# Performance work log

Hardware: AMD Instinct MI355X
Metric: run time of the kernel (lower is better)

The kernel has to match this reference:

```python
import jax, jax.numpy as jnp
import numpy as np
from jax import lax

N, D = 32768, 512
N_Q, BINS = 8, 2048


def setup_inputs() -> dict:
    key = jax.random.key(0)
    k1, k2 = jax.random.split(key)
    hidden_states = jax.random.normal(k1, (N, D), dtype=jnp.float32)
    # learned codebooks: n_q stages, each [BINS, D] (bins list clamps to one size)
    codebooks = jax.random.normal(k2, (N_Q, BINS, D), dtype=jnp.float32)
    return {"hidden_states": hidden_states, "codebooks": codebooks}


def reference(hidden_states, codebooks):
    """ResidualVectorQuantizer.encode: sequential residual VQ over n_q codebooks.

    Distances sum((r - c)^2) computed via the GEMM expansion
    ||r||^2 - 2 r.c^T + ||c||^2 (same math, matmul-friendly).
    Returns (codes [n_q, N] int, quantized [N, D]).
    """
    cb_sq = jnp.sum(codebooks * codebooks, axis=-1)  # [n_q, bins]

    def step(carry, stage):
        residual, quantized = carry
        cb, csq = stage  # [bins, D], [bins]
        r_sq = jnp.sum(residual * residual, axis=-1, keepdims=True)  # [N, 1]
        dist = r_sq - 2.0 * (residual @ cb.T) + csq[None, :]  # [N, bins]
        idx = jnp.argmin(dist, axis=-1)  # [N]
        chosen = cb[idx]  # [N, D]
        return (residual - chosen, quantized + chosen), idx

    init = (hidden_states, jnp.zeros_like(hidden_states))
    (_, quantized), codes = lax.scan(step, init, (codebooks, cb_sq))
    return codes, quantized
```

## Files before the change

kernel.cpp:

```cpp
#include <hip/hip_runtime.h>
#include <hip/hip_bf16.h>

#define NROWS 32768
#define DIM   512
#define NQ    8
#define NBINS 2048

#define MARGIN 1.0f

typedef __attribute__((ext_vector_type(8))) short short8v;
typedef __attribute__((ext_vector_type(4))) float f32x4;

__device__ inline unsigned short f2bf(float x) {
    __hip_bfloat16 h = __float2bfloat16(x);
    return *reinterpret_cast<unsigned short*>(&h);
}

typedef __attribute__((address_space(3))) void lds_t;
typedef __attribute__((address_space(1))) const void gbl_t;
__device__ inline void gload16(const void* g, void* l) {
    __builtin_amdgcn_global_load_lds((gbl_t*)g, (lds_t*)l, 16, 0, 0);
}

__device__ inline float pw_combine(float s) {
#pragma unroll
    for (int m = 1; m <= 16; m <<= 1) {
        float o = __shfl_xor(s, m, 64);
        s = __fadd_rn(s, o);
    }
    return s;
}

__global__ __launch_bounds__(256) void k_prep(const float* __restrict__ cb,
                                              unsigned short* __restrict__ o,
                                              float* __restrict__ csq32) {
    int row = blockIdx.x * 4 + (threadIdx.x >> 6);
    int lane = threadIdx.x & 63;
    const float* cp = cb + (size_t)row * DIM;

    float4 a = *(const float4*)(cp + lane * 8);
    float4 b = *(const float4*)(cp + lane * 8 + 4);
    short8v v;
    v[0] = f2bf(a.x); v[1] = f2bf(a.y); v[2] = f2bf(a.z); v[3] = f2bf(a.w);
    v[4] = f2bf(b.x); v[5] = f2bf(b.y); v[6] = f2bf(b.z); v[7] = f2bf(b.w);
    *(short8v*)(o + (size_t)row * DIM + lane * 8) = v;

    float s = 0.0f;
    if (lane < 32) {
        int base = (lane >> 3) * 128 + (lane & 7);
        float e = cp[base];
        s = __fmul_rn(e, e);
#pragma unroll
        for (int m = 1; m < 16; ++m) {
            float e2 = cp[base + 8 * m];
            s = __fadd_rn(s, __fmul_rn(e2, e2));
        }
    }
    s = pw_combine(s);
    if (lane == 0) csq32[row] = s;
}

__global__ __launch_bounds__(128) void k_init(const float* __restrict__ h,
                                              float* __restrict__ rout,
                                              float* __restrict__ rsq,
                                              unsigned short* __restrict__ ahi) {
    int row = blockIdx.x;
    int t = threadIdx.x;
    __shared__ float sq[DIM];
    float4 r = *(const float4*)(h + (size_t)row * DIM + t * 4);
    *(float4*)(rout + (size_t)row * DIM + t * 4) = r;
    ushort4 hv;
    hv.x = f2bf(r.x); hv.y = f2bf(r.y); hv.z = f2bf(r.z); hv.w = f2bf(r.w);
    *(ushort4*)(ahi + (size_t)row * DIM + t * 4) = hv;
    sq[t * 4 + 0] = __fmul_rn(r.x, r.x);
    sq[t * 4 + 1] = __fmul_rn(r.y, r.y);
    sq[t * 4 + 2] = __fmul_rn(r.z, r.z);
    sq[t * 4 + 3] = __fmul_rn(r.w, r.w);
    __syncthreads();
    if (t < 32) {
        int base = (t >> 3) * 128 + (t & 7);
        float s = sq[base];
#pragma unroll
        for (int m = 1; m < 16; ++m) s = __fadd_rn(s, sq[base + 8 * m]);
        s = pw_combine(s);
        if (t == 0) rsq[row] = s;
    }
}

__global__ __launch_bounds__(256, 4) void k_gemm(const unsigned short* __restrict__ Ahi,
                                                 const unsigned short* __restrict__ Bcb,
                                                 const float* __restrict__ csq,
                                                 float* __restrict__ partD,
                                                 int* __restrict__ partI) {
    __shared__ __align__(16) char lds[33792];
    __shared__ float csqS[128];

    const int tid = threadIdx.x;
    const int lane = tid & 63;
    const int w = tid >> 6;
    const int wr = w >> 1;
    const int wc = w & 1;

    const int wg = blockIdx.x;
    const int rem = wg & 255;
    const int panel = (rem & 7) * 32 + (rem >> 3);
    const int T = wg >> 8;

    if (tid < 128) csqS[tid] = csq[T * 128 + tid];

    const char* Abase = (const char*)(Ahi + (size_t)panel * 128 * DIM);
    const char* Bbase = (const char*)(Bcb + (size_t)T * 128 * DIM);

    int goff[4], loff[4];
#pragma unroll
    for (int i = 0; i < 4; ++i) {
        int L = i * 256 + tid;
        int row = L >> 3, cc = L & 7;
        goff[i] = row * (DIM * 2) + ((cc ^ (row & 7)) << 4);
        loff[i] = L * 16;
    }

    f32x4 acc[4][4];
#pragma unroll
    for (int m = 0; m < 4; ++m)
#pragma unroll
        for (int n = 0; n < 4; ++n) acc[m][n] = (f32x4){0.f, 0.f, 0.f, 0.f};

#pragma unroll
    for (int ks = 0; ks < 8; ++ks) {
        __syncthreads();
        const int k0b = ks * 128;
#pragma unroll
        for (int i = 0; i < 4; ++i) {
            gload16(Abase + goff[i] + k0b, lds + loff[i]);
            gload16(Bbase + goff[i] + k0b, lds + 16384 + loff[i]);
        }
        __syncthreads();
        __builtin_amdgcn_s_setprio(1);
        const char* Ab = lds;
        const char* Bb = lds + 16384;
#pragma unroll
        for (int kk = 0; kk < 2; ++kk) {
            const int sw = (((kk * 4 + (lane >> 4)) ^ (lane & 7)) << 4);
            short8v bF[4];
#pragma unroll
            for (int n = 0; n < 4; ++n) {
                int rowB = wc * 64 + n * 16 + (lane & 15);
                bF[n] = *(const short8v*)(Bb + rowB * 128 + sw);
            }
#pragma unroll
            for (int m = 0; m < 4; ++m) {
                int rowA = wr * 64 + m * 16 + (lane & 15);
                short8v aF = *(const short8v*)(Ab + rowA * 128 + sw);
#pragma unroll
                for (int n = 0; n < 4; ++n)
                    acc[m][n] = __builtin_amdgcn_mfma_f32_16x16x32_bf16(
                        aF, bF[n], acc[m][n], 0, 0, 0);
            }
        }
        __builtin_amdgcn_s_setprio(0);
    }

    float td0 = 3.4e38f, td1 = 3.4e38f, td2 = 3.4e38f, td3 = 3.4e38f;
    int ti0 = 0, ti1 = 0, ti2 = 0, ti3 = 0;
    float* distf = (float*)lds;
    const int row2 = tid >> 1, h = tid & 1;

#pragma unroll
    for (int p = 0; p < 2; ++p) {
        __syncthreads();
        if (wc == p) {
#pragma unroll
            for (int m = 0; m < 4; ++m)
#pragma unroll
                for (int n = 0; n < 4; ++n)
#pragma unroll
                    for (int r = 0; r < 4; ++r) {
                        int row = wr * 64 + m * 16 + (lane >> 4) * 4 + r;
                        int cl = n * 16 + (lane & 15);
                        distf[row * 66 + cl] = csqS[p * 64 + cl] - 2.0f * acc[m][n][r];
                    }
        }
        __syncthreads();
        int binb = T * 128 + p * 64 + h * 32;
        for (int c = 0; c < 32; ++c) {
            float d = distf[row2 * 66 + h * 32 + c];
            int bin = binb + c;
            if (d < td3) {
                if (d < td2) {
                    td3 = td2; ti3 = ti2;
                    if (d < td1) {
                        td2 = td1; ti2 = ti1;
                        if (d < td0) { td1 = td0; ti1 = ti0; td0 = d; ti0 = bin; }
                        else { td1 = d; ti1 = bin; }
                    } else { td2 = d; ti2 = bin; }
                } else { td3 = d; ti3 = bin; }
            }
        }
    }
#pragma unroll
    for (int j = 0; j < 4; ++j) {
        float d = __shfl_xor(j == 0 ? td0 : (j == 1 ? td1 : (j == 2 ? td2 : td3)), 1);
        int bin = __shfl_xor(j == 0 ? ti0 : (j == 1 ? ti1 : (j == 2 ? ti2 : ti3)), 1);
        if (d < td3) {
            if (d < td2) {
                td3 = td2; ti3 = ti2;
                if (d < td1) {
                    td2 = td1; ti2 = ti1;
                    if (d < td0) { td1 = td0; ti1 = ti0; td0 = d; ti0 = bin; }
                    else { td1 = d; ti1 = bin; }
                } else { td2 = d; ti2 = bin; }
            } else { td3 = d; ti3 = bin; }
        }
    }
    if (h == 0) {
        size_t g = ((size_t)panel * 128 + row2) * 64 + T * 4;
        partD[g + 0] = td0; partI[g + 0] = ti0;
        partD[g + 1] = td1; partI[g + 1] = ti1;
        partD[g + 2] = td2; partI[g + 2] = ti2;
        partD[g + 3] = td3; partI[g + 3] = ti3;
    }
}

__global__ __launch_bounds__(128) void k_ru(const float* __restrict__ partD,
                                            const int* __restrict__ partI,
                                            float* __restrict__ resid,
                                            float* __restrict__ rsq,
                                            const float* __restrict__ csq,
                                            const float* __restrict__ cb,
                                            float* __restrict__ codeOut,
                                            unsigned short* __restrict__ ahi,
                                            const float* __restrict__ hidden,
                                            int last) {
    const int row = blockIdx.x;
    const int t = threadIdx.x;
    __shared__ int sIdx;
    __shared__ float sq[DIM];

    if (t < 64) {
        float d = partD[(size_t)row * 64 + t];
        int bi0 = partI[(size_t)row * 64 + t];

        float bd = d; int bix = bi0;
#pragma unroll
        for (int o = 32; o > 0; o >>= 1) {
            float od = __shfl_xor(bd, o);
            int oi = __shfl_xor(bix, o);
            if (od < bd || (od == bd && oi < bix)) { bd = od; bix = oi; }
        }
        bool cand = (d <= bd + MARGIN);
        unsigned long long mask = __ballot(cand);
        int winI;
        if (__popcll(mask) == 1) {
            winI = bix;
        } else {
            float myD = 3.4e38f; int myI = 0x7fffffff;
            if (cand) {
                const float* rp = resid + (size_t)row * DIM;
                const float* cp = cb + (size_t)bi0 * DIM;
                float acc = 0.0f;
                for (int k = 0; k < DIM; k += 4) {
                    float4 rv = *(const float4*)(rp + k);
                    float4 cv = *(const float4*)(cp + k);
                    acc = fmaf(rv.x, cv.x, acc);
                    acc = fmaf(rv.y, cv.y, acc);
                    acc = fmaf(rv.z, cv.z, acc);
                    acc = fmaf(rv.w, cv.w, acc);
                }
                myD = __fadd_rn(__fsub_rn(rsq[row], __fmul_rn(2.0f, acc)), csq[bi0]);
                myI = bi0;
            }
#pragma unroll
            for (int o = 32; o > 0; o >>= 1) {
                float od = __shfl_xor(myD, o);
                int oi = __shfl_xor(myI, o);
                if (od < myD || (od == myD && oi < myI)) { myD = od; myI = oi; }
            }
            winI = myI;
        }
        if (t == 0) {
            sIdx = winI;
            codeOut[row] = (float)winI;
        }
    }
    __syncthreads();
    const int id = sIdx;

    float4 r = *(const float4*)(resid + (size_t)row * DIM + t * 4);
    float4 c = *(const float4*)(cb + (size_t)id * DIM + t * 4);
    r.x = __fsub_rn(r.x, c.x);
    r.y = __fsub_rn(r.y, c.y);
    r.z = __fsub_rn(r.z, c.z);
    r.w = __fsub_rn(r.w, c.w);

    if (last) {
        float4 hv4 = *(const float4*)(hidden + (size_t)row * DIM + t * 4);
        float4 q;
        q.x = __fsub_rn(hv4.x, r.x);
        q.y = __fsub_rn(hv4.y, r.y);
        q.z = __fsub_rn(hv4.z, r.z);
        q.w = __fsub_rn(hv4.w, r.w);
        *(float4*)(resid + (size_t)row * DIM + t * 4) = q;
        return;
    }

    *(float4*)(resid + (size_t)row * DIM + t * 4) = r;
    ushort4 hv;
    hv.x = f2bf(r.x); hv.y = f2bf(r.y); hv.z = f2bf(r.z); hv.w = f2bf(r.w);
    *(ushort4*)(ahi + (size_t)row * DIM + t * 4) = hv;

    sq[t * 4 + 0] = __fmul_rn(r.x, r.x);
    sq[t * 4 + 1] = __fmul_rn(r.y, r.y);
    sq[t * 4 + 2] = __fmul_rn(r.z, r.z);
    sq[t * 4 + 3] = __fmul_rn(r.w, r.w);
    __syncthreads();
    if (t < 32) {
        int base = (t >> 3) * 128 + (t & 7);
        float s = sq[base];
#pragma unroll
        for (int m = 1; m < 16; ++m) s = __fadd_rn(s, sq[base + 8 * m]);
        s = pw_combine(s);
        if (t == 0) rsq[row] = s;
    }
}

extern "C" void kernel_launch(void* const* d_in, const int* in_sizes, int n_in,
                              void* d_out, int out_size, void* d_ws, size_t ws_size,
                              hipStream_t stream) {
    const float* hidden = (const float*)d_in[0];
    const float* cbs = (const float*)d_in[1];

    float* out_codes = (float*)d_out;
    float* resid = out_codes + (size_t)NQ * NROWS;

    unsigned short* Ahi = (unsigned short*)d_ws;
    unsigned short* Cbf = Ahi + (size_t)NROWS * DIM;
    float* csq32 = (float*)(Cbf + (size_t)NQ * NBINS * DIM);
    float* rsq = csq32 + (size_t)NQ * NBINS;
    float* partD = rsq + NROWS;
    int* partI = (int*)(partD + (size_t)NROWS * 64);

    k_prep<<<NQ * NBINS / 4, 256, 0, stream>>>(cbs, Cbf, csq32);
    k_init<<<NROWS, 128, 0, stream>>>(hidden, resid, rsq, Ahi);

    for (int s = 0; s < NQ; ++s) {
        const float* cbS = cbs + (size_t)s * NBINS * DIM;
        k_gemm<<<(NROWS / 128) * (NBINS / 128), 256, 0, stream>>>(
            Ahi, Cbf + (size_t)s * NBINS * DIM, csq32 + (size_t)s * NBINS,
            partD, partI);
        k_ru<<<NROWS, 128, 0, stream>>>(partD, partI, resid, rsq,
                                        csq32 + (size_t)s * NBINS, cbS,
                                        out_codes + (size_t)s * NROWS, Ahi,
                                        hidden, s == NQ - 1);
    }
}
```

Measured before the change: 1.219 ms.

## Remap GEMM workgroup order and process one row per wavefront in update kernel

The GEMM block-index mapping is changed so each group of consecutive workgroups covers a 16-panel by 16-codebook-tile region, which should improve L2 reuse of the A panels and B tiles. The residual-update kernel now gives each 64-lane wavefront a whole row (4 rows per 256-thread block) instead of one 128-thread block per row. This removes the shared-memory index broadcast and the first block barrier, and the residual load is issued early so it overlaps the argmin reduction. Each lane now handles 8 elements with wider bf16 stores. The rsq reduction keeps the same summation order, so results should be unchanged.

```diff
diff --git a/kernel.cpp b/kernel.cpp
--- a/kernel.cpp
+++ b/kernel.cpp
@@ -102,9 +102,9 @@
     const int wc = w & 1;
 
     const int wg = blockIdx.x;
-    const int rem = wg & 255;
-    const int panel = (rem & 7) * 32 + (rem >> 3);
-    const int T = wg >> 8;
+    const int seq = wg >> 3;
+    const int panel = (wg & 7) * 32 + (seq >> 8) * 16 + (seq & 15);
+    const int T = (seq >> 4) & 15;
 
     if (tid < 128) csqS[tid] = csq[T * 128 + tid];
 
@@ -222,7 +222,7 @@
     }
 }
 
-__global__ __launch_bounds__(128) void k_ru(const float* __restrict__ partD,
+__global__ __launch_bounds__(256) void k_ru(const float* __restrict__ partD,
                                             const int* __restrict__ partI,
                                             float* __restrict__ resid,
                                             float* __restrict__ rsq,
@@ -232,95 +232,110 @@
                                             unsigned short* __restrict__ ahi,
                                             const float* __restrict__ hidden,
                                             int last) {
-    const int row = blockIdx.x;
-    const int t = threadIdx.x;
-    __shared__ int sIdx;
-    __shared__ float sq[DIM];
-
-    if (t < 64) {
-        float d = partD[(size_t)row * 64 + t];
-        int bi0 = partI[(size_t)row * 64 + t];
-
-        float bd = d; int bix = bi0;
+    const int w = threadIdx.x >> 6;
+    const int lane = threadIdx.x & 63;
+    const int row = blockIdx.x * 4 + w;
+    __shared__ float sq[4][DIM];
+
+    const float* rp = resid + (size_t)row * DIM;
+    float4 r0 = *(const float4*)(rp + lane * 8);
+    float4 r1 = *(const float4*)(rp + lane * 8 + 4);
+
+    float d = partD[(size_t)row * 64 + lane];
+    int bi0 = partI[(size_t)row * 64 + lane];
+    float bd = d; int bix = bi0;
+#pragma unroll
+    for (int o = 32; o > 0; o >>= 1) {
+        float od = __shfl_xor(bd, o);
+        int oi = __shfl_xor(bix, o);
+        if (od < bd || (od == bd && oi < bix)) { bd = od; bix = oi; }
+    }
+    bool cand = (d <= bd + MARGIN);
+    unsigned long long mask = __ballot(cand);
+    int winI;
+    if (__popcll(mask) == 1) {
+        winI = bix;
+    } else {
+        float myD = 3.4e38f; int myI = 0x7fffffff;
+        if (cand) {
+            const float* cp = cb + (size_t)bi0 * DIM;
+            float acc = 0.0f;
+            for (int k = 0; k < DIM; k += 4) {
+                float4 rv = *(const float4*)(rp + k);
+                float4 cv = *(const float4*)(cp + k);
+                acc = fmaf(rv.x, cv.x, acc);
+                acc = fmaf(rv.y, cv.y, acc);
+                acc = fmaf(rv.z, cv.z, acc);
+                acc = fmaf(rv.w, cv.w, acc);
+            }
+            myD = __fadd_rn(__fsub_rn(rsq[row], __fmul_rn(2.0f, acc)), csq[bi0]);
+            myI = bi0;
+        }
 #pragma unroll
         for (int o = 32; o > 0; o >>= 1) {
-            float od = __shfl_xor(bd, o);
-            int oi = __shfl_xor(bix, o);
-            if (od < bd || (od == bd && oi < bix)) { bd = od; bix = oi; }
-        }
-        bool cand = (d <= bd + MARGIN);
-        unsigned long long mask = __ballot(cand);
-        int winI;
-        if (__popcll(mask) == 1) {
-            winI = bix;
-        } else {
-            float myD = 3.4e38f; int myI = 0x7fffffff;
-            if (cand) {
-                const float* rp = resid + (size_t)row * DIM;
-                const float* cp = cb + (size_t)bi0 * DIM;
-                float acc = 0.0f;
-                for (int k = 0; k < DIM; k += 4) {
-                    float4 rv = *(const float4*)(rp + k);
-                    float4 cv = *(const float4*)(cp + k);
-                    acc = fmaf(rv.x, cv.x, acc);
-                    acc = fmaf(rv.y, cv.y, acc);
-                    acc = fmaf(rv.z, cv.z, acc);
-                    acc = fmaf(rv.w, cv.w, acc);
-                }
-                myD = __fadd_rn(__fsub_rn(rsq[row], __fmul_rn(2.0f, acc)), csq[bi0]);
-                myI = bi0;
-            }
-#pragma unroll
-            for (int o = 32; o > 0; o >>= 1) {
-                float od = __shfl_xor(myD, o);
-                int oi = __shfl_xor(myI, o);
-                if (od < myD || (od == myD && oi < myI)) { myD = od; myI = oi; }
-            }
-            winI = myI;
-        }
-        if (t == 0) {
-            sIdx = winI;
-            codeOut[row] = (float)winI;
-        }
-    }
+            float od = __shfl_xor(myD, o);
+            int oi = __shfl_xor(myI, o);
+            if (od < myD || (od == myD && oi < myI)) { myD = od; myI = oi; }
+        }
+        winI = myI;
+    }
+    if (lane == 0) codeOut[row] = (float)winI;
+    const int id = winI;
+
+    const float* cp8 = cb + (size_t)id * DIM + lane * 8;
+    float4 c0 = *(const float4*)cp8;
+    float4 c1 = *(const float4*)(cp8 + 4);
+    r0.x = __fsub_rn(r0.x, c0.x);
+    r0.y = __fsub_rn(r0.y, c0.y);
+    r0.z = __fsub_rn(r0.z, c0.z);
+    r0.w = __fsub_rn(r0.w, c0.w);
+    r1.x = __fsub_rn(r1.x, c1.x);
+    r1.y = __fsub_rn(r1.y, c1.y);
+    r1.z = __fsub_rn(r1.z, c1.z);
+    r1.w = __fsub_rn(r1.w, c1.w);
+
+    float* wp = resid + (size_t)row * DIM + lane * 8;
+    if (last) {
+        const float* hp = hidden + (size_t)row * DIM + lane * 8;
+        float4 h0 = *(const float4*)hp;
+        float4 h1 = *(const float4*)(hp + 4);
+        float4 q0, q1;
+        q0.x = __fsub_rn(h0.x, r0.x);
+        q0.y = __fsub_rn(h0.y, r0.y);
+        q0.z = __fsub_rn(h0.z, r0.z);
+        q0.w = __fsub_rn(h0.w, r0.w);
+        q1.x = __fsub_rn(h1.x, r1.x);
+        q1.y = __fsub_rn(h1.y, r1.y);
+        q1.z = __fsub_rn(h1.z, r1.z);
+        q1.w = __fsub_rn(h1.w, r1.w);
+        *(float4*)wp = q0;
+        *(float4*)(wp + 4) = q1;
+        return;
+    }
+
+    *(float4*)wp = r0;
+    *(float4*)(wp + 4) = r1;
+    short8v hv;
+    hv[0] = f2bf(r0.x); hv[1] = f2bf(r0.y); hv[2] = f2bf(r0.z); hv[3] = f2bf(r0.w);
+    hv[4] = f2bf(r1.x); hv[5] = f2bf(r1.y); hv[6] = f2bf(r1.z); hv[7] = f2bf(r1.w);
+    *(short8v*)(ahi + (size_t)row * DIM + lane * 8) = hv;
+
+    sq[w][lane * 8 + 0] = __fmul_rn(r0.x, r0.x);
+    sq[w][lane * 8 + 1] = __fmul_rn(r0.y, r0.y);
+    sq[w][lane * 8 + 2] = __fmul_rn(r0.z, r0.z);
+    sq[w][lane * 8 + 3] = __fmul_rn(r0.w, r0.w);
+    sq[w][lane * 8 + 4] = __fmul_rn(r1.x, r1.x);
+    sq[w][lane * 8 + 5] = __fmul_rn(r1.y, r1.y);
+    sq[w][lane * 8 + 6] = __fmul_rn(r1.z, r1.z);
+    sq[w][lane * 8 + 7] = __fmul_rn(r1.w, r1.w);
     __syncthreads();
-    const int id = sIdx;
-
-    float4 r = *(const float4*)(resid + (size_t)row * DIM + t * 4);
-    float4 c = *(const float4*)(cb + (size_t)id * DIM + t * 4);
-    r.x = __fsub_rn(r.x, c.x);
-    r.y = __fsub_rn(r.y, c.y);
-    r.z = __fsub_rn(r.z, c.z);
-    r.w = __fsub_rn(r.w, c.w);
-
-    if (last) {
-        float4 hv4 = *(const float4*)(hidden + (size_t)row * DIM + t * 4);
-        float4 q;
-        q.x = __fsub_rn(hv4.x, r.x);
-        q.y = __fsub_rn(hv4.y, r.y);
-        q.z = __fsub_rn(hv4.z, r.z);
-        q.w = __fsub_rn(hv4.w, r.w);
-        *(float4*)(resid + (size_t)row * DIM + t * 4) = q;
-        return;
-    }
-
-    *(float4*)(resid + (size_t)row * DIM + t * 4) = r;
-    ushort4 hv;
-    hv.x = f2bf(r.x); hv.y = f2bf(r.y); hv.z = f2bf(r.z); hv.w = f2bf(r.w);
-    *(ushort4*)(ahi + (size_t)row * DIM + t * 4) = hv;
-
-    sq[t * 4 + 0] = __fmul_rn(r.x, r.x);
-    sq[t * 4 + 1] = __fmul_rn(r.y, r.y);
-    sq[t * 4 + 2] = __fmul_rn(r.z, r.z);
-    sq[t * 4 + 3] = __fmul_rn(r.w, r.w);
-    __syncthreads();
-    if (t < 32) {
-        int base = (t >> 3) * 128 + (t & 7);
-        float s = sq[base];
-#pragma unroll
-        for (int m = 1; m < 16; ++m) s = __fadd_rn(s, sq[base + 8 * m]);
+    if (lane < 32) {
+        int base = (lane >> 3) * 128 + (lane & 7);
+        float s = sq[w][base];
+#pragma unroll
+        for (int m = 1; m < 16; ++m) s = __fadd_rn(s, sq[w][base + 8 * m]);
         s = pw_combine(s);
-        if (t == 0) rsq[row] = s;
+        if (lane == 0) rsq[row] = s;
     }
 }
 
@@ -348,9 +363,9 @@
         k_gemm<<<(NROWS / 128) * (NBINS / 128), 256, 0, stream>>>(
             Ahi, Cbf + (size_t)s * NBINS * DIM, csq32 + (size_t)s * NBINS,
             partD, partI);
-        k_ru<<<NROWS, 128, 0, stream>>>(partD, partI, resid, rsq,
-                                        csq32 + (size_t)s * NBINS, cbS,
-                                        out_codes + (size_t)s * NROWS, Ahi,
-                                        hidden, s == NQ - 1);
-    }
-}
+        k_ru<<<NROWS / 4, 256, 0, stream>>>(partD, partI, resid, rsq,
+                                            csq32 + (size_t)s * NBINS, cbS,
+                                            out_codes + (size_t)s * NROWS, Ahi,
+                                            hidden, s == NQ - 1);
+    }
+}
```

Measured after the change: 1.243 ms. About the same (+2.0%).
